# Performance work log

Hardware: AMD Instinct MI355X
Metric: run time of the kernel (lower is better)

The kernel has to match this reference:

```python
import jax, jax.numpy as jnp
import numpy as np

EPS = 1e-5

def _layernorm(x, g, b):
    m = jnp.mean(x, axis=-1, keepdims=True)
    v = jnp.mean((x - m) ** 2, axis=-1, keepdims=True)
    return (x - m) * jax.lax.rsqrt(v + EPS) * g + b

def setup_inputs() -> dict:
    key = jax.random.key(0)
    ks = jax.random.split(key, 6)
    B, N, D, H, F = 4, 4096, 256, 256, 1024
    s = lambda d: 1.0 / np.sqrt(d)
    return {
        "x": jax.random.normal(ks[0], (B, N, D), jnp.float32),
        "ln1_g": jnp.ones((D,), jnp.float32),
        "ln1_b": jnp.zeros((D,), jnp.float32),
        "wq": jax.random.normal(ks[1], (D, H), jnp.float32) * s(D),
        "bq": jnp.zeros((H,), jnp.float32),
        "wk": jax.random.normal(ks[2], (D, H), jnp.float32) * s(D),
        "bk": jnp.zeros((H,), jnp.float32),
        "wv": jax.random.normal(ks[3], (D, D), jnp.float32) * s(D),
        "bv": jnp.zeros((D,), jnp.float32),
        "ln2_g": jnp.ones((D,), jnp.float32),
        "ln2_b": jnp.zeros((D,), jnp.float32),
        "w1": jax.random.normal(ks[4], (D, F), jnp.float32) * s(D),
        "b1": jnp.zeros((F,), jnp.float32),
        "w2": jax.random.normal(ks[5], (F, D), jnp.float32) * s(F),
        "b2": jnp.zeros((D,), jnp.float32),
    }

def reference(x, ln1_g, ln1_b, wq, bq, wk, bk, wv, bv, ln2_g, ln2_b, w1, b1, w2, b2):
    hdim = wq.shape[1]
    x = _layernorm(x, ln1_g, ln1_b)                      # [B,N,D]
    q = x @ wq + bq                                      # [B,N,H]
    k = x @ wk + bk                                      # [B,N,H]
    v = x @ wv + bv                                      # [B,N,D]
    att = jnp.einsum('bnh,bmh->bnm', q, k) / jnp.sqrt(jnp.float32(hdim))
    att = jax.nn.softmax(att, axis=-1)                   # [B,N,N]
    x = jnp.einsum('bnm,bmd->bnd', att, v) + x           # residual around attention
    h = _layernorm(x, ln2_g, ln2_b)
    h = jax.nn.relu(h @ w1 + b1) @ w2 + b2
    return h + x
```

## Files before the change

kernel.cpp:

```cpp
#include <hip/hip_runtime.h>
#include <stdint.h>

typedef unsigned short u16;
typedef __attribute__((ext_vector_type(8))) short short8;
typedef __attribute__((ext_vector_type(4))) float f32x4;
typedef __attribute__((ext_vector_type(16))) float f32x16;

__device__ __forceinline__ u16 f2b(float f){
  union { float f; unsigned u; } x; x.f = f;
  unsigned r = x.u + 0x7FFFu + ((x.u >> 16) & 1u);
  return (u16)(r >> 16);
}

__device__ __forceinline__ unsigned cvtpk_bf16(float lo, float hi){
  unsigned r;
  asm("v_cvt_pk_bf16_f32 %0, %1, %2" : "=v"(r) : "v"(lo), "v"(hi));
  return r;
}

__device__ __forceinline__ void gload_lds16(const void* g, void* l){
  __builtin_amdgcn_global_load_lds(
      (const __attribute__((address_space(1))) unsigned int*)g,
      (__attribute__((address_space(3))) unsigned int*)l, 16, 0, 0);
}

__global__ void __launch_bounds__(256) transpose_cast(const float* __restrict__ in,
                                                      u16* __restrict__ out, int K, int N){
  __shared__ float sm[32][33];
  int k0 = blockIdx.x*32, n0 = blockIdx.y*32;
  int t = threadIdx.x; int tr = t>>5, tc = t&31;
  #pragma unroll
  for (int p=0;p<4;p++) sm[p*8+tr][tc] = in[(size_t)(k0+p*8+tr)*N + n0+tc];
  __syncthreads();
  #pragma unroll
  for (int p=0;p<4;p++) out[(size_t)(n0+p*8+tr)*K + k0+tc] = f2b(sm[tc][p*8+tr]);
}

__global__ void __launch_bounds__(256) transpose_cast3(const float* __restrict__ wq,
                                                       const float* __restrict__ wk,
                                                       const float* __restrict__ wv,
                                                       u16* __restrict__ out){
  __shared__ float sm[32][33];
  int z = blockIdx.z;
  const float* in = (z==0) ? wq : (z==1) ? wk : wv;
  u16* o = out + (size_t)z*65536;
  int k0 = blockIdx.x*32, n0 = blockIdx.y*32;
  int t = threadIdx.x; int tr = t>>5, tc = t&31;
  #pragma unroll
  for (int p=0;p<4;p++) sm[p*8+tr][tc] = in[(size_t)(k0+p*8+tr)*256 + n0+tc];
  __syncthreads();
  #pragma unroll
  for (int p=0;p<4;p++) o[(size_t)(n0+p*8+tr)*256 + k0+tc] = f2b(sm[tc][p*8+tr]);
}

__global__ void __launch_bounds__(256) ln_kernel(const float* __restrict__ in,
                                                 const float* __restrict__ g,
                                                 const float* __restrict__ bb,
                                                 float* __restrict__ outF,
                                                 u16* __restrict__ outB){
  int row = blockIdx.x, t = threadIdx.x;
  size_t base = (size_t)row*256;
  float v = in[base + t];
  float s = v;
  #pragma unroll
  for (int m=1;m<64;m<<=1) s += __shfl_xor(s, m);
  __shared__ float red[4];
  int w = t>>6;
  if ((t&63)==0) red[w] = s;
  __syncthreads();
  float mean = (red[0]+red[1]+red[2]+red[3]) * (1.0f/256.0f);
  float d = v - mean;
  float s2 = d*d;
  #pragma unroll
  for (int m=1;m<64;m<<=1) s2 += __shfl_xor(s2, m);
  __syncthreads();
  if ((t&63)==0) red[w] = s2;
  __syncthreads();
  float var = (red[0]+red[1]+red[2]+red[3]) * (1.0f/256.0f);
  float y = d * rsqrtf(var + 1e-5f) * g[t] + bb[t];
  if (outF) outF[base+t] = y;
  outB[base+t] = f2b(y);
}

template<int MODE>
__global__ void __launch_bounds__(256, 2) gemm_bt(const u16* __restrict__ A,
                                                  const u16* __restrict__ BT,
                                                  const float* __restrict__ bias,
                                                  const float* __restrict__ bias2,
                                                  const float* __restrict__ bias3,
                                                  const float* __restrict__ res,
                                                  float* __restrict__ outF,
                                                  u16* __restrict__ outB,
                                                  u16* __restrict__ outB2,
                                                  u16* __restrict__ outB3,
                                                  int M, int N, int K){
  __shared__ u16 As[128*64];
  __shared__ u16 Bs[128*64];
  int tid = threadIdx.x;
  int m0 = blockIdx.x*128, n0 = blockIdx.y*128;
  int wave = tid>>6, lane = tid&63, lr = lane&15, lg = lane>>4;
  int wm = (wave>>1)*64, wn = (wave&1)*64;

  f32x4 acc[4][4];
  #pragma unroll
  for (int i=0;i<4;i++)
    #pragma unroll
    for (int j=0;j<4;j++) acc[i][j] = (f32x4){0.f,0.f,0.f,0.f};

  int nk = K >> 6;
  for (int kt=0; kt<nk; ++kt){
    __syncthreads();
    #pragma unroll
    for (int i=0;i<4;i++){
      int de = i*256 + tid; int row = de>>3; int ch = de&7; int sc = ch ^ (row&7);
      gload_lds16(A + (size_t)(m0+row)*K + kt*64 + sc*8, (char*)As + de*16);
    }
    #pragma unroll
    for (int i=0;i<4;i++){
      int de = i*256 + tid; int row = de>>3; int ch = de&7; int sc = ch ^ (row&7);
      gload_lds16(BT + (size_t)(n0+row)*K + kt*64 + sc*8, (char*)Bs + de*16);
    }
    asm volatile("s_waitcnt vmcnt(0)" ::: "memory");
    __syncthreads();
    #pragma unroll
    for (int kk=0;kk<2;kk++){
      short8 af[4], bf[4];
      #pragma unroll
      for (int mi=0;mi<4;mi++){
        int row = wm + mi*16 + lr;
        int c = (kk*4 + lg) ^ (row&7);
        af[mi] = *(const short8*)&As[row*64 + c*8];
      }
      #pragma unroll
      for (int ni=0;ni<4;ni++){
        int row = wn + ni*16 + lr;
        int c = (kk*4 + lg) ^ (row&7);
        bf[ni] = *(const short8*)&Bs[row*64 + c*8];
      }
      #pragma unroll
      for (int mi=0;mi<4;mi++)
        #pragma unroll
        for (int ni=0;ni<4;ni++)
          acc[mi][ni] = __builtin_amdgcn_mfma_f32_16x16x32_bf16(af[mi], bf[ni], acc[mi][ni], 0,0,0);
    }
  }
  #pragma unroll
  for (int mi=0;mi<4;mi++)
    #pragma unroll
    for (int ni=0;ni<4;ni++)
      #pragma unroll
      for (int r=0;r<4;r++){
        int row = m0 + wm + mi*16 + lg*4 + r;
        int col = n0 + wn + ni*16 + lr;
        if (MODE==3){
          int seg = n0 >> 8;
          int c2 = col & 255;
          float bb = (seg==0) ? bias[c2] : (seg==1) ? bias2[c2] : bias3[c2];
          float vout = acc[mi][ni][r] + bb;
          if (seg==0)      outB [(size_t)row*256 + c2] = f2b(vout);
          else if (seg==1) outB2[(size_t)row*256 + c2] = f2b(vout);
          else {
            size_t gaddr = ((size_t)(row>>12)<<20)
                         + ((((size_t)((row&4095)>>3)<<8) + (size_t)c2)<<3) + (row&7);
            outB3[gaddr] = f2b(vout);
          }
        } else {
          float vout = acc[mi][ni][r] + bias[col];
          if (MODE==1) vout = fmaxf(vout, 0.f);
          if (MODE==2) outF[(size_t)row*N + col] = vout + res[(size_t)row*N + col];
          else         outB[(size_t)row*N + col] = f2b(vout);
        }
      }
}

__device__ __forceinline__ void stage_tiles(const u16* __restrict__ Kb,
                                            const u16* __restrict__ Vt,
                                            int b, int kv0,
                                            char* Kdst, char* Vdst, int tid){
  #pragma unroll
  for (int i=0;i<4;i++){
    int de = i*256 + tid; int kv = de>>5; int c = de&31; int sc = c ^ (kv&7);
    gload_lds16(Kb + (((size_t)(b*4096 + kv0 + kv))<<8) + sc*8, Kdst + (size_t)de*16);
  }
  #pragma unroll
  for (int i=0;i<4;i++){
    int de = i*256 + tid; int kvc = de>>8; int d = de&255;
    gload_lds16(Vt + ((((size_t)b*512 + (kv0>>3) + kvc)<<8) + (size_t)d)*8,
                Vdst + (size_t)de*16);
  }
}

__global__ void __launch_bounds__(256, 2) flash_attn32(const u16* __restrict__ Qb,
                                                       const u16* __restrict__ Kb,
                                                       const u16* __restrict__ Vt,
                                                       u16* __restrict__ Opart,
                                                       float* __restrict__ MLpart){
  __shared__ __align__(16) char smem[75776];
  const int NC = 4096;
  int tid = threadIdx.x, wave = tid>>6, lane = tid&63;
  int lq = lane & 31, hi = lane >> 5;
  int b = blockIdx.y, s = blockIdx.z;
  int qb0 = blockIdx.x*128 + wave*32;
  int kvbeg = s*1024;
  const int NT = 32;
  u16* PsW = (u16*)(smem + 65536) + wave*32*40;

  short8 qf[16];
  {
    const u16* qbase = Qb + (((size_t)b*NC + qb0 + lq)<<8) + hi*8;
    #pragma unroll
    for (int ks=0; ks<16; ks++) qf[ks] = *(const short8*)(qbase + ks*16);
  }

  f32x16 o[8];
  #pragma unroll
  for (int i=0;i<8;i++)
    o[i] = (f32x16){0.f,0.f,0.f,0.f,0.f,0.f,0.f,0.f,0.f,0.f,0.f,0.f,0.f,0.f,0.f,0.f};
  float mrun = -__builtin_inff(), ell = 0.f;

  stage_tiles(Kb, Vt, b, kvbeg, smem, smem + 16384, tid);
  asm volatile("s_waitcnt vmcnt(0)" ::: "memory");
  __syncthreads();

  for (int t=0; t<NT; t++){
    char* Kc = smem + ((t&1) ? 32768 : 0);
    char* Vc = Kc + 16384;
    char* Kn = smem + ((t&1) ? 0 : 32768);
    char* Vn = Kn + 16384;
    int kv0 = kvbeg + t*32;
    if (t+1 < NT) stage_tiles(Kb, Vt, b, kv0+32, Kn, Vn, tid);

    f32x16 sacc = (f32x16){0.f,0.f,0.f,0.f,0.f,0.f,0.f,0.f,0.f,0.f,0.f,0.f,0.f,0.f,0.f,0.f};
    __builtin_amdgcn_s_setprio(1);
    #pragma unroll
    for (int ks=0; ks<16; ks++){
      int c = ks*2 + hi;
      short8 kf = *(const short8*)(Kc + lq*512 + ((c ^ (lq&7))<<4));
      sacc = __builtin_amdgcn_mfma_f32_32x32x16_bf16(kf, qf[ks], sacc, 0,0,0);
    }
    __builtin_amdgcn_s_setprio(0);

    float tmax = sacc[0];
    #pragma unroll
    for (int r=1;r<16;r++) tmax = fmaxf(tmax, sacc[r]);
    tmax *= 0.0625f;
    tmax = fmaxf(tmax, __shfl_xor(tmax, 32));
    if (!__all(tmax <= mrun + 8.f)){
      float mn = fmaxf(mrun, tmax);
      float sc = __expf(mrun - mn);
      mrun = mn; ell *= sc;
      #pragma unroll
      for (int r=0;r<16;r++){
        float scr = __shfl(sc, (r&3)+8*(r>>2)+4*hi);
        #pragma unroll
        for (int dt=0; dt<8; dt++) o[dt][r] *= scr;
      }
    }

    float rs = 0.f;
    #pragma unroll
    for (int h=0; h<2; h++){
      float p[8];
      #pragma unroll
      for (int r=0;r<8;r++){ p[r] = __expf(sacc[h*8+r]*0.0625f - mrun); rs += p[r]; }
      uint2 w0, w1;
      w0.x = cvtpk_bf16(p[0], p[1]);  w0.y = cvtpk_bf16(p[2], p[3]);
      w1.x = cvtpk_bf16(p[4], p[5]);  w1.y = cvtpk_bf16(p[6], p[7]);
      *(uint2*)(PsW + lq*40 + h*16 + hi*4)     = w0;
      *(uint2*)(PsW + lq*40 + h*16 + 8 + hi*4) = w1;
    }
    rs += __shfl_xor(rs, 32);
    ell += rs;
    asm volatile("s_waitcnt lgkmcnt(0)" ::: "memory");
    __builtin_amdgcn_sched_barrier(0);
    short8 pa0 = *(const short8*)(PsW + lq*40 + hi*8);
    short8 pa1 = *(const short8*)(PsW + lq*40 + 16 + hi*8);

    __builtin_amdgcn_s_setprio(1);
    #pragma unroll
    for (int dt=0; dt<8; dt++){
      short8 vf0 = *(const short8*)(Vc + (((hi  )*256 + dt*32 + lq)<<4));
      short8 vf1 = *(const short8*)(Vc + (((2+hi)*256 + dt*32 + lq)<<4));
      o[dt] = __builtin_amdgcn_mfma_f32_32x32x16_bf16(pa0, vf0, o[dt], 0,0,0);
      o[dt] = __builtin_amdgcn_mfma_f32_32x32x16_bf16(pa1, vf1, o[dt], 0,0,0);
    }
    __builtin_amdgcn_s_setprio(0);

    asm volatile("s_waitcnt vmcnt(0)" ::: "memory");
    __syncthreads();
  }

  size_t rowb = (size_t)s*16384 + (size_t)b*NC + qb0;
  #pragma unroll
  for (int dt=0; dt<8; dt++)
    #pragma unroll
    for (int r=0;r<16;r++){
      int q = (r&3) + 8*(r>>2) + 4*hi;
      Opart[(rowb + q)*256 + dt*32 + lq] = f2b(o[dt][r]);
    }
  if (lane < 32){
    MLpart[(rowb + lane)*2]     = mrun;
    MLpart[(rowb + lane)*2 + 1] = ell;
  }
}

__global__ void __launch_bounds__(256) merge4_ln(const u16* __restrict__ Opart,
                                                 const float* __restrict__ MLpart,
                                                 const float* __restrict__ xln,
                                                 const float* __restrict__ g2,
                                                 const float* __restrict__ be2,
                                                 float* __restrict__ x2,
                                                 u16* __restrict__ h2){
  int row = blockIdx.x; int t = threadIdx.x;
  const size_t RS = 16384ull*256;
  float m[4], l[4];
  #pragma unroll
  for (int s=0;s<4;s++){
    m[s] = MLpart[((size_t)s*16384 + row)*2];
    l[s] = MLpart[((size_t)s*16384 + row)*2 + 1];
  }
  float M = fmaxf(fmaxf(m[0],m[1]), fmaxf(m[2],m[3]));
  float e[4]; float den = 0.f;
  #pragma unroll
  for (int s=0;s<4;s++){ e[s] = __expf(m[s]-M); den += l[s]*e[s]; }
  float inv = 1.0f/den;
  size_t idx = (size_t)row*256 + t;
  float v = 0.f;
  #pragma unroll
  for (int s=0;s<4;s++){
    unsigned u = Opart[(size_t)s*RS + idx];
    v += __uint_as_float(u << 16) * e[s];
  }
  v = v*inv + xln[idx];
  x2[idx] = v;
  float s1 = v;
  #pragma unroll
  for (int mk=1;mk<64;mk<<=1) s1 += __shfl_xor(s1, mk);
  __shared__ float red[4];
  int w = t>>6;
  if ((t&63)==0) red[w] = s1;
  __syncthreads();
  float mean = (red[0]+red[1]+red[2]+red[3]) * (1.0f/256.0f);
  float d = v - mean;
  float s2 = d*d;
  #pragma unroll
  for (int mk=1;mk<64;mk<<=1) s2 += __shfl_xor(s2, mk);
  __syncthreads();
  if ((t&63)==0) red[w] = s2;
  __syncthreads();
  float var = (red[0]+red[1]+red[2]+red[3]) * (1.0f/256.0f);
  h2[idx] = f2b(d * rsqrtf(var + 1e-5f) * g2[t] + be2[t]);
}

extern "C" void kernel_launch(void* const* d_in, const int* in_sizes, int n_in,
                              void* d_out, int out_size, void* d_ws, size_t ws_size,
                              hipStream_t stream){
  const float* x   = (const float*)d_in[0];
  const float* g1  = (const float*)d_in[1];
  const float* be1 = (const float*)d_in[2];
  const float* wq  = (const float*)d_in[3];
  const float* bq  = (const float*)d_in[4];
  const float* wk  = (const float*)d_in[5];
  const float* bk  = (const float*)d_in[6];
  const float* wv  = (const float*)d_in[7];
  const float* bv  = (const float*)d_in[8];
  const float* g2  = (const float*)d_in[9];
  const float* be2 = (const float*)d_in[10];
  const float* w1  = (const float*)d_in[11];
  const float* bm1 = (const float*)d_in[12];
  const float* w2  = (const float*)d_in[13];
  const float* bm2 = (const float*)d_in[14];
  float* out = (float*)d_out;

  const size_t RS = 16384ull*256;
  char* p = (char*)d_ws;
  float* xln = (float*)p;  p += RS*4;
  u16*  Op   = (u16*)p;    p += 4*RS*2;
  float* ML  = (float*)p;  p += 4*16384ull*2*4;
  u16* xb  = (u16*)p; p += RS*2;
  u16* qb  = (u16*)p; p += RS*2;
  u16* kb  = (u16*)p; p += RS*2;
  u16* vT  = (u16*)p; p += RS*2;
  u16* wqkvT = (u16*)p; p += 3*65536ull*2;
  u16* w1T = (u16*)p; p += 262144ull*2;
  u16* w2T = (u16*)p; p += 262144ull*2;
  float* x2 = xln;
  u16*   h1 = Op;
  u16*   h2 = qb;

  transpose_cast3<<<dim3(8,8,3), 256,0,stream>>>(wq, wk, wv, wqkvT);
  transpose_cast<<<dim3(8,32), 256,0,stream>>>(w1, w1T, 256, 1024);
  transpose_cast<<<dim3(32,8), 256,0,stream>>>(w2, w2T, 1024, 256);

  ln_kernel<<<16384,256,0,stream>>>(x, g1, be1, xln, xb);

  gemm_bt<3><<<dim3(128,6),256,0,stream>>>(xb, wqkvT, bq, bk, bv, nullptr, nullptr,
                                           qb, kb, vT, 16384,768,256);

  flash_attn32<<<dim3(32,4,4),256,0,stream>>>(qb, kb, vT, Op, ML);
  merge4_ln<<<16384,256,0,stream>>>(Op, ML, xln, g2, be2, x2, h2);

  gemm_bt<1><<<dim3(128,8),256,0,stream>>>(h2, w1T, bm1, nullptr, nullptr, nullptr, nullptr,
                                           h1, nullptr, nullptr, 16384,1024,256);
  gemm_bt<2><<<dim3(128,2),256,0,stream>>>(h1, w2T, bm2, nullptr, nullptr, x2, out,
                                           nullptr, nullptr, nullptr, 16384,256,1024);
}
```

Measured before the change: 173.2 us.

## Load V fragments directly from global memory and merge weight transposes into one launch

The flash attention kernel no longer stages V tiles through LDS. Each wave reads its V MFMA fragments straight from global memory with a one-step software prefetch across the dt loop, which shrinks LDS from about 74KB to 42KB and halves the staging traffic. The three weight transpose-cast launches are merged into a single 704-block kernel to cut launch overhead. The risk is that V reads now have global latency and are repeated by every wave in the block instead of being shared through LDS, so the PV MFMAs may stall on memory.

```diff
diff --git a/kernel.cpp b/kernel.cpp
--- a/kernel.cpp
+++ b/kernel.cpp
@@ -24,33 +24,33 @@
       (__attribute__((address_space(3))) unsigned int*)l, 16, 0, 0);
 }
 
-__global__ void __launch_bounds__(256) transpose_cast(const float* __restrict__ in,
-                                                      u16* __restrict__ out, int K, int N){
+__global__ void __launch_bounds__(256) transpose_all(const float* __restrict__ wq,
+                                                     const float* __restrict__ wk,
+                                                     const float* __restrict__ wv,
+                                                     const float* __restrict__ w1,
+                                                     const float* __restrict__ w2,
+                                                     u16* __restrict__ wqkvT,
+                                                     u16* __restrict__ w1T,
+                                                     u16* __restrict__ w2T){
   __shared__ float sm[32][33];
-  int k0 = blockIdx.x*32, n0 = blockIdx.y*32;
+  int id = blockIdx.x;
+  const float* in; u16* out; int K, N, kx, ny;
+  if (id < 192){
+    int j = id >> 6, r = id & 63;
+    in = (j==0) ? wq : (j==1) ? wk : wv;
+    out = wqkvT + (size_t)j*65536; K = 256; N = 256; kx = r>>3; ny = r&7;
+  } else if (id < 448){
+    int r = id - 192; in = w1; out = w1T; K = 256; N = 1024; kx = r&7; ny = r>>3;
+  } else {
+    int r = id - 448; in = w2; out = w2T; K = 1024; N = 256; kx = r>>3; ny = r&7;
+  }
+  int k0 = kx*32, n0 = ny*32;
   int t = threadIdx.x; int tr = t>>5, tc = t&31;
   #pragma unroll
   for (int p=0;p<4;p++) sm[p*8+tr][tc] = in[(size_t)(k0+p*8+tr)*N + n0+tc];
   __syncthreads();
   #pragma unroll
   for (int p=0;p<4;p++) out[(size_t)(n0+p*8+tr)*K + k0+tc] = f2b(sm[tc][p*8+tr]);
-}
-
-__global__ void __launch_bounds__(256) transpose_cast3(const float* __restrict__ wq,
-                                                       const float* __restrict__ wk,
-                                                       const float* __restrict__ wv,
-                                                       u16* __restrict__ out){
-  __shared__ float sm[32][33];
-  int z = blockIdx.z;
-  const float* in = (z==0) ? wq : (z==1) ? wk : wv;
-  u16* o = out + (size_t)z*65536;
-  int k0 = blockIdx.x*32, n0 = blockIdx.y*32;
-  int t = threadIdx.x; int tr = t>>5, tc = t&31;
-  #pragma unroll
-  for (int p=0;p<4;p++) sm[p*8+tr][tc] = in[(size_t)(k0+p*8+tr)*256 + n0+tc];
-  __syncthreads();
-  #pragma unroll
-  for (int p=0;p<4;p++) o[(size_t)(n0+p*8+tr)*256 + k0+tc] = f2b(sm[tc][p*8+tr]);
 }
 
 __global__ void __launch_bounds__(256) ln_kernel(const float* __restrict__ in,
@@ -173,20 +173,12 @@
       }
 }
 
-__device__ __forceinline__ void stage_tiles(const u16* __restrict__ Kb,
-                                            const u16* __restrict__ Vt,
-                                            int b, int kv0,
-                                            char* Kdst, char* Vdst, int tid){
+__device__ __forceinline__ void stage_K(const u16* __restrict__ Kb,
+                                        int b, int kv0, char* Kdst, int tid){
   #pragma unroll
   for (int i=0;i<4;i++){
     int de = i*256 + tid; int kv = de>>5; int c = de&31; int sc = c ^ (kv&7);
     gload_lds16(Kb + (((size_t)(b*4096 + kv0 + kv))<<8) + sc*8, Kdst + (size_t)de*16);
-  }
-  #pragma unroll
-  for (int i=0;i<4;i++){
-    int de = i*256 + tid; int kvc = de>>8; int d = de&255;
-    gload_lds16(Vt + ((((size_t)b*512 + (kv0>>3) + kvc)<<8) + (size_t)d)*8,
-                Vdst + (size_t)de*16);
   }
 }
 
@@ -195,7 +187,7 @@
                                                        const u16* __restrict__ Vt,
                                                        u16* __restrict__ Opart,
                                                        float* __restrict__ MLpart){
-  __shared__ __align__(16) char smem[75776];
+  __shared__ __align__(16) char smem[43008];
   const int NC = 4096;
   int tid = threadIdx.x, wave = tid>>6, lane = tid&63;
   int lq = lane & 31, hi = lane >> 5;
@@ -203,7 +195,7 @@
   int qb0 = blockIdx.x*128 + wave*32;
   int kvbeg = s*1024;
   const int NT = 32;
-  u16* PsW = (u16*)(smem + 65536) + wave*32*40;
+  u16* PsW = (u16*)(smem + 32768) + wave*32*40;
 
   short8 qf[16];
   {
@@ -212,23 +204,24 @@
     for (int ks=0; ks<16; ks++) qf[ks] = *(const short8*)(qbase + ks*16);
   }
 
+  const u16* vbase0 = Vt + (((size_t)b*512 + (kvbeg>>3) + hi    )<<11) + lq*8;
+  const u16* vbase1 = Vt + (((size_t)b*512 + (kvbeg>>3) + 2 + hi)<<11) + lq*8;
+
   f32x16 o[8];
   #pragma unroll
   for (int i=0;i<8;i++)
     o[i] = (f32x16){0.f,0.f,0.f,0.f,0.f,0.f,0.f,0.f,0.f,0.f,0.f,0.f,0.f,0.f,0.f,0.f};
   float mrun = -__builtin_inff(), ell = 0.f;
 
-  stage_tiles(Kb, Vt, b, kvbeg, smem, smem + 16384, tid);
+  stage_K(Kb, b, kvbeg, smem, tid);
   asm volatile("s_waitcnt vmcnt(0)" ::: "memory");
   __syncthreads();
 
   for (int t=0; t<NT; t++){
-    char* Kc = smem + ((t&1) ? 32768 : 0);
-    char* Vc = Kc + 16384;
-    char* Kn = smem + ((t&1) ? 0 : 32768);
-    char* Vn = Kn + 16384;
+    char* Kc = smem + ((t&1)<<14);
+    char* Kn = smem + (((t+1)&1)<<14);
     int kv0 = kvbeg + t*32;
-    if (t+1 < NT) stage_tiles(Kb, Vt, b, kv0+32, Kn, Vn, tid);
+    if (t+1 < NT) stage_K(Kb, b, kv0+32, Kn, tid);
 
     f32x16 sacc = (f32x16){0.f,0.f,0.f,0.f,0.f,0.f,0.f,0.f,0.f,0.f,0.f,0.f,0.f,0.f,0.f,0.f};
     __builtin_amdgcn_s_setprio(1);
@@ -271,6 +264,12 @@
     }
     rs += __shfl_xor(rs, 32);
     ell += rs;
+
+    const u16* v0p = vbase0 + (size_t)t*8192;
+    const u16* v1p = vbase1 + (size_t)t*8192;
+    short8 vf0 = *(const short8*)(v0p);
+    short8 vf1 = *(const short8*)(v1p);
+
     asm volatile("s_waitcnt lgkmcnt(0)" ::: "memory");
     __builtin_amdgcn_sched_barrier(0);
     short8 pa0 = *(const short8*)(PsW + lq*40 + hi*8);
@@ -279,10 +278,14 @@
     __builtin_amdgcn_s_setprio(1);
     #pragma unroll
     for (int dt=0; dt<8; dt++){
-      short8 vf0 = *(const short8*)(Vc + (((hi  )*256 + dt*32 + lq)<<4));
-      short8 vf1 = *(const short8*)(Vc + (((2+hi)*256 + dt*32 + lq)<<4));
+      short8 nf0, nf1;
+      if (dt < 7){
+        nf0 = *(const short8*)(v0p + (dt+1)*256);
+        nf1 = *(const short8*)(v1p + (dt+1)*256);
+      }
       o[dt] = __builtin_amdgcn_mfma_f32_32x32x16_bf16(pa0, vf0, o[dt], 0,0,0);
       o[dt] = __builtin_amdgcn_mfma_f32_32x32x16_bf16(pa1, vf1, o[dt], 0,0,0);
+      vf0 = nf0; vf1 = nf1;
     }
     __builtin_amdgcn_s_setprio(0);
 
@@ -388,9 +391,7 @@
   u16*   h1 = Op;
   u16*   h2 = qb;
 
-  transpose_cast3<<<dim3(8,8,3), 256,0,stream>>>(wq, wk, wv, wqkvT);
-  transpose_cast<<<dim3(8,32), 256,0,stream>>>(w1, w1T, 256, 1024);
-  transpose_cast<<<dim3(32,8), 256,0,stream>>>(w2, w2T, 1024, 256);
+  transpose_all<<<704, 256, 0, stream>>>(wq, wk, wv, w1, w2, wqkvT, w1T, w2T);
 
   ln_kernel<<<16384,256,0,stream>>>(x, g1, be1, xln, xb);
 
```

Measured after the change: 255.1 us. 47.3% more time.
